# Performance work log

Measured on AMD Instinct MI355X. Metric: run time of the kernel, lower is better.

The kernel has to match this reference:

```python
import jax, jax.numpy as jnp
import numpy as np

N, E, DIN, DH, DOUT = 50000, 800000, 128, 128, 64


def setup_inputs() -> dict:
    key = jax.random.key(0)
    ks = jax.random.split(key, 10)
    s = 0.05  # keep activations numerically sane
    return {
        "x": jax.random.normal(ks[0], (N, DIN), jnp.float32),
        "edge_index": jax.random.randint(ks[1], (2, E), 0, N, jnp.int64),
        "w_in": jax.random.normal(ks[2], (DIN, DH), jnp.float32) * s,
        "b_in": jnp.zeros((DH,), jnp.float32),
        "w_l0": jax.random.normal(ks[3], (DH, DH), jnp.float32) * s,
        "w_r0": jax.random.normal(ks[4], (DH, DH), jnp.float32) * s,
        "b0": jnp.zeros((DH,), jnp.float32),
        "w_l1": jax.random.normal(ks[5], (DH, DH), jnp.float32) * s,
        "w_r1": jax.random.normal(ks[6], (DH, DH), jnp.float32) * s,
        "b1": jnp.zeros((DH,), jnp.float32),
        "w_l2": jax.random.normal(ks[7], (DH, DOUT), jnp.float32) * s,
        "w_r2": jax.random.normal(ks[8], (DH, DOUT), jnp.float32) * s,
        "b2": jnp.zeros((DOUT,), jnp.float32),
    }


def _sage_conv(x, src, dst, w_l, w_r, b, n_nodes):
    # PyG SAGEConv (mean aggr): out = lin_l(mean_{j in N(i)} x_j) + lin_r(x_i)
    msg = x[src]  # [E, d] gather
    agg = jax.ops.segment_sum(msg, dst, num_segments=n_nodes)
    deg = jax.ops.segment_sum(jnp.ones((src.shape[0],), x.dtype), dst, num_segments=n_nodes)
    agg = agg / jnp.maximum(deg, 1.0)[:, None]  # isolated nodes -> 0
    return agg @ w_l + x @ w_r + b


def reference(x, edge_index, w_in, b_in, w_l0, w_r0, b0, w_l1, w_r1, b1, w_l2, w_r2, b2):
    src, dst = edge_index[0], edge_index[1]
    n = x.shape[0]
    h = x @ w_in + b_in
    inp = h
    h = jax.nn.relu(h)
    # conv 0 (hidden->hidden) + relu + (eval dropout = id) + residual
    h = _sage_conv(h, src, dst, w_l0, w_r0, b0, n)
    h = jax.nn.relu(h) + 0.2 * inp
    # conv 1 (hidden->hidden)
    h = _sage_conv(h, src, dst, w_l1, w_r1, b1, n)
    h = jax.nn.relu(h) + 0.2 * inp
    # conv 2 (hidden->out), no activation/residual
    h = _sage_conv(h, src, dst, w_l2, w_r2, b2, n)
    return jax.nn.log_softmax(h, axis=-1)
```

## Files before the change

### kernel.cpp

```cpp
#include <hip/hip_runtime.h>
#include <stdint.h>

#define NN 50000
#define NE 800000
#define NBIN 196
#define ABLK 196
#define EPB 4082
#define BCAP 6144
#define NRT 3125
#define GRID_LIN 1024

typedef __attribute__((ext_vector_type(8))) short short8;
typedef __attribute__((ext_vector_type(4))) float floatx4;

__device__ __forceinline__ uint16_t f2bf(float f){
  union { float f; uint32_t u; } c; c.f = f;
  uint32_t u = c.u + 0x7FFFu + ((c.u >> 16) & 1u);
  return (uint16_t)(u >> 16);
}
__device__ __forceinline__ float bflo(uint32_t v){
  union { uint32_t u; float f; } c; c.u = v << 16; return c.f;
}
__device__ __forceinline__ float bfhi(uint32_t v){
  union { uint32_t u; float f; } c; c.u = v & 0xFFFF0000u; return c.f;
}

#define B_HIST ABLK
#define B_PIN 64
#define B_P0  128
#define B_P1  128
#define B_P2  64

__device__ __forceinline__ void pack_one(int idx, const float* __restrict__ wl,
                                         const float* __restrict__ wr,
                                         uint16_t* __restrict__ bp,
                                         int ncolL, int ncolR, int NT){
  int j = idx & 7, lane = (idx >> 3) & 63, rest = idx >> 9;
  int nt = rest % NT, kt = rest / NT;
  int k = kt * 32 + ((lane >> 4) << 3) + j;
  int n = nt * 16 + (lane & 15);
  float v = (n < ncolL) ? wl[k * ncolL + n] : wr[k * ncolR + (n - ncolL)];
  bp[idx] = f2bf(v);
}

__global__ __launch_bounds__(256) void k_prep(const int* __restrict__ ei, int* __restrict__ histC,
                                              const float* __restrict__ w_in,
                                              const float* __restrict__ w_l0, const float* __restrict__ w_r0,
                                              const float* __restrict__ w_l1, const float* __restrict__ w_r1,
                                              const float* __restrict__ w_l2, const float* __restrict__ w_r2,
                                              uint16_t* __restrict__ bpIn, uint16_t* __restrict__ bp0,
                                              uint16_t* __restrict__ bp1, uint16_t* __restrict__ bp2){
  __shared__ int hsh[NBIN];
  int b = blockIdx.x;
  if (b < B_HIST){
    for (int i = threadIdx.x; i < NBIN; i += 256) hsh[i] = 0;
    __syncthreads();
    int base = b * EPB;
    for (int k = threadIdx.x; k < EPB; k += 256){
      int e = base + k;
      if (e < NE) atomicAdd(&hsh[ei[NE + e] >> 8], 1);
    }
    __syncthreads();
    for (int i = threadIdx.x; i < NBIN; i += 256) histC[b * NBIN + i] = hsh[i];
    return;
  }
  b -= B_HIST;
  if (b < B_PIN){ pack_one(b * 256 + threadIdx.x, w_in, w_in, bpIn, 128, 0, 8); return; }
  b -= B_PIN;
  if (b < B_P0){ pack_one(b * 256 + threadIdx.x, w_l0, w_r0, bp0, 128, 128, 16); return; }
  b -= B_P0;
  if (b < B_P1){ pack_one(b * 256 + threadIdx.x, w_l1, w_r1, bp1, 128, 128, 16); return; }
  b -= B_P1;
  pack_one(b * 256 + threadIdx.x, w_l2, w_r2, bp2, 64, 64, 8);
}

__global__ __launch_bounds__(256) void k_scanS1(const int* __restrict__ histC, int* __restrict__ histE,
                                                int* __restrict__ colTot){
  __shared__ int s[256];
  int t = blockIdx.x;
  int b = threadIdx.x;
  int v = (b < ABLK) ? histC[b * NBIN + t] : 0;
  s[b] = v;
  __syncthreads();
  #pragma unroll
  for (int off = 1; off < 256; off <<= 1){
    int u = (b >= off) ? s[b - off] : 0;
    __syncthreads();
    s[b] += u;
    __syncthreads();
  }
  if (b < ABLK) histE[b * NBIN + t] = s[b] - v;
  if (b == ABLK - 1) colTot[t] = s[b];
}

__global__ __launch_bounds__(256) void k_scanS2(const int* __restrict__ colTot, int* __restrict__ binStart){
  __shared__ int s[256];
  int t = threadIdx.x;
  int tot = (t < NBIN) ? colTot[t] : 0;
  s[t] = tot;
  __syncthreads();
  #pragma unroll
  for (int off = 1; off < 256; off <<= 1){
    int u = (t >= off) ? s[t - off] : 0;
    __syncthreads();
    s[t] += u;
    __syncthreads();
  }
  if (t < NBIN) binStart[t] = s[t] - tot;
  if (t == 0) binStart[NBIN] = NE;
}

#define B_BIN 196
#define SMSZ 20488

__global__ __launch_bounds__(256) void k_mid(const int* __restrict__ ei,
                                             const int* __restrict__ histC, const int* __restrict__ histE,
                                             const int* __restrict__ binStart,
                                             uint32_t* __restrict__ pairs,
                                             const float* __restrict__ x,
                                             const uint16_t* __restrict__ BpIn, const float* __restrict__ b_in,
                                             const uint16_t* __restrict__ Bp0, const float* __restrict__ b0,
                                             uint16_t* __restrict__ resb, uint16_t* __restrict__ y0,
                                             uint16_t* __restrict__ z0){
  __shared__ __align__(16) char smraw[SMSZ];
  int t = threadIdx.x;
  if (blockIdx.x < B_BIN){
    int* loc = (int*)smraw;
    int* cur = loc + NBIN;
    int* gof = cur + NBIN;
    int* sc  = gof + NBIN + NBIN;
    uint32_t* st = (uint32_t*)(sc + 256);
    int b = blockIdx.x;
    int cv = (t < NBIN) ? histC[b * NBIN + t] : 0;
    sc[t] = cv;
    __syncthreads();
    #pragma unroll
    for (int off = 1; off < 256; off <<= 1){
      int u = (t >= off) ? sc[t - off] : 0;
      __syncthreads();
      sc[t] += u;
      __syncthreads();
    }
    if (t < NBIN){
      int excl = sc[t] - cv;
      loc[t] = excl;
      cur[t] = excl;
      gof[t] = binStart[t] + histE[b * NBIN + t];
    }
    __syncthreads();
    int base = b * EPB;
    for (int k = t; k < EPB; k += 256){
      int e = base + k;
      if (e < NE){
        int d = ei[NE + e];
        int s0 = ei[e];
        int pos = atomicAdd(&cur[d >> 8], 1);
        st[pos] = (uint32_t)s0 | ((uint32_t)d << 16);
      }
    }
    __syncthreads();
    int cnt = min(EPB, NE - base);
    for (int k = t; k < cnt; k += 256){
      uint32_t v = st[k];
      int bin = (int)(v >> 24);
      pairs[gof[bin] + (k - loc[bin])] = v;
    }
    return;
  }
  uint16_t* ash = (uint16_t*)smraw;
  int lane = t & 63, wave = t >> 6;
  short8 bIn[4][2], bC0[4][4];
  #pragma unroll
  for (int kt = 0; kt < 4; ++kt){
    #pragma unroll
    for (int n = 0; n < 2; ++n)
      bIn[kt][n] = *(const short8*)(BpIn + (size_t)((kt * 8 + wave * 2 + n) * 64 + lane) * 8);
    #pragma unroll
    for (int n = 0; n < 4; ++n)
      bC0[kt][n] = *(const short8*)(Bp0 + (size_t)((kt * 16 + wave * 4 + n) * 64 + lane) * 8);
  }
  int m = lane & 15, quad = lane >> 4;
  for (int rt = blockIdx.x - B_BIN; rt < NRT; rt += GRID_LIN){
    int r0 = rt * 16;
    const float* xrow = x + (size_t)(r0 + m) * 128 + quad * 8;
    short8 af[4];
    #pragma unroll
    for (int kt = 0; kt < 4; ++kt){
      float4 p = *(const float4*)(xrow + kt * 32);
      float4 q2 = *(const float4*)(xrow + kt * 32 + 4);
      short8 a;
      a[0] = (short)f2bf(p.x);  a[1] = (short)f2bf(p.y);
      a[2] = (short)f2bf(p.z);  a[3] = (short)f2bf(p.w);
      a[4] = (short)f2bf(q2.x); a[5] = (short)f2bf(q2.y);
      a[6] = (short)f2bf(q2.z); a[7] = (short)f2bf(q2.w);
      af[kt] = a;
    }
    floatx4 accH[2];
    #pragma unroll
    for (int n = 0; n < 2; ++n) accH[n] = (floatx4){0.f, 0.f, 0.f, 0.f};
    #pragma unroll
    for (int kt = 0; kt < 4; ++kt)
      #pragma unroll
      for (int n = 0; n < 2; ++n)
        accH[n] = __builtin_amdgcn_mfma_f32_16x16x32_bf16(af[kt], bIn[kt][n], accH[n], 0, 0, 0);
    int rbase = r0 + quad * 4;
    __syncthreads();
    #pragma unroll
    for (int n = 0; n < 2; ++n){
      int c = (wave * 2 + n) * 16 + m;
      float bi = b_in[c];
      #pragma unroll
      for (int i = 0; i < 4; ++i){
        float hh = accH[n][i] + bi;
        int row = rbase + i;
        resb[(size_t)row * 128 + c] = f2bf(0.2f * hh);
        ash[(quad * 4 + i) * 136 + c] = f2bf(fmaxf(hh, 0.f));
      }
    }
    __syncthreads();
    short8 af2[4];
    #pragma unroll
    for (int kt = 0; kt < 4; ++kt)
      af2[kt] = *(const short8*)&ash[m * 136 + quad * 8 + kt * 32];
    floatx4 acc[4];
    #pragma unroll
    for (int n = 0; n < 4; ++n) acc[n] = (floatx4){0.f, 0.f, 0.f, 0.f};
    #pragma unroll
    for (int kt = 0; kt < 4; ++kt)
      #pragma unroll
      for (int n = 0; n < 4; ++n)
        acc[n] = __builtin_amdgcn_mfma_f32_16x16x32_bf16(af2[kt], bC0[kt][n], acc[n], 0, 0, 0);
    #pragma unroll
    for (int n = 0; n < 4; ++n){
      int c = (wave * 4 + n) * 16 + m;
      #pragma unroll
      for (int i = 0; i < 4; ++i){
        float v = acc[n][i];
        int row = rbase + i;
        if (c < 128) y0[(size_t)row * 128 + c] = f2bf(v);
        else         z0[(size_t)row * 128 + (c - 128)] = f2bf(v + b0[c - 128]);
      }
    }
  }
}

__global__ __launch_bounds__(256) void k_csr(const uint32_t* __restrict__ pairs, const int* __restrict__ binStart,
                                             int* __restrict__ rowp, uint16_t* __restrict__ colx){
  __shared__ uint32_t pl[BCAP];
  __shared__ uint16_t stg[BCAP];
  __shared__ int h[256], sc[256];
  int i = blockIdx.x, t = threadIdx.x;
  int p0 = binStart[i], p1 = binStart[i + 1];
  int cnt = min(p1 - p0, BCAP);
  for (int k = t; k < cnt; k += 256) pl[k] = pairs[p0 + k];
  h[t] = 0;
  __syncthreads();
  for (int k = t; k < cnt; k += 256) atomicAdd(&h[(pl[k] >> 16) & 255], 1);
  __syncthreads();
  int cv = h[t];
  sc[t] = cv;
  __syncthreads();
  #pragma unroll
  for (int off = 1; off < 256; off <<= 1){
    int u = (t >= off) ? sc[t - off] : 0;
    __syncthreads();
    sc[t] += u;
    __syncthreads();
  }
  int excl = sc[t] - cv;
  int n0 = i << 8;
  int nc = min(256, NN - n0);
  if (t < nc) rowp[n0 + t] = p0 + excl;
  if (i == NBIN - 1 && t == 0) rowp[NN] = NE;
  h[t] = excl;
  __syncthreads();
  for (int k = t; k < cnt; k += 256){
    uint32_t v = pl[k];
    int pos = atomicAdd(&h[(v >> 16) & 255], 1);
    stg[pos] = (uint16_t)(v & 0xFFFFu);
  }
  __syncthreads();
  for (int k = t; k < cnt; k += 256) colx[p0 + k] = stg[k];
}

template<int NTW, int MODE>
__global__ __launch_bounds__(256) void k_gemm(const uint16_t* __restrict__ A, const uint16_t* __restrict__ Bp,
                                              const float* __restrict__ bias,
                                              uint16_t* __restrict__ o0, uint16_t* __restrict__ o1,
                                              float* __restrict__ o2){
  const int NTT = 4 * NTW;
  int lane = threadIdx.x & 63;
  int wave = threadIdx.x >> 6;
  short8 bfrag[4][NTW];
  #pragma unroll
  for (int kt = 0; kt < 4; ++kt)
    #pragma unroll
    for (int n = 0; n < NTW; ++n)
      bfrag[kt][n] = *(const short8*)(Bp + (size_t)((kt * NTT + wave * NTW + n) * 64 + lane) * 8);

  int m = lane & 15, quad = lane >> 4;
  const int nrt = NN / 16;
  for (int rt = blockIdx.x; rt < nrt; rt += gridDim.x){
    int r0 = rt * 16;
    const uint16_t* arow = A + (size_t)(r0 + m) * 128 + quad * 8;
    short8 af[4];
    #pragma unroll
    for (int kt = 0; kt < 4; ++kt) af[kt] = *(const short8*)(arow + kt * 32);
    floatx4 acc[NTW];
    #pragma unroll
    for (int n = 0; n < NTW; ++n) acc[n] = (floatx4){0.f, 0.f, 0.f, 0.f};
    #pragma unroll
    for (int kt = 0; kt < 4; ++kt)
      #pragma unroll
      for (int n = 0; n < NTW; ++n)
        acc[n] = __builtin_amdgcn_mfma_f32_16x16x32_bf16(af[kt], bfrag[kt][n], acc[n], 0, 0, 0);

    int rbase = r0 + quad * 4;
    #pragma unroll
    for (int n = 0; n < NTW; ++n){
      int c = (wave * NTW + n) * 16 + m;
      #pragma unroll
      for (int i = 0; i < 4; ++i){
        float v = acc[n][i];
        int row = rbase + i;
        if (MODE == 1){
          if (c < 128) o0[(size_t)row * 128 + c] = f2bf(v);
          else         o1[(size_t)row * 128 + (c - 128)] = f2bf(v + bias[c - 128]);
        } else {
          if (c < 64) o0[(size_t)row * 64 + c] = f2bf(v);
          else        o2[(size_t)row * 64 + (c - 64)] = v + bias[c - 64];
        }
      }
    }
  }
}

__global__ __launch_bounds__(256) void agg_mid(const uint4* __restrict__ yb, const uint4* __restrict__ zb,
                                               const uint4* __restrict__ resb,
                                               const uint16_t* __restrict__ colx, const int* __restrict__ rowp,
                                               uint4* __restrict__ hb_out){
  int wid = blockIdx.x * 4 + (threadIdx.x >> 6);
  if (wid >= NN) return;
  int lane = threadIdx.x & 63;
  int q = lane >> 4, sub = lane & 15;
  int e0 = rowp[wid], e1 = rowp[wid + 1];
  float a0 = 0.f, a1 = 0.f, a2 = 0.f, a3 = 0.f, a4 = 0.f, a5 = 0.f, a6 = 0.f, a7 = 0.f;
  int e = e0 + q;
  for (; e + 12 < e1; e += 16){
    uint4 v0 = yb[(size_t)colx[e]      * 16 + sub];
    uint4 v1 = yb[(size_t)colx[e + 4]  * 16 + sub];
    uint4 v2 = yb[(size_t)colx[e + 8]  * 16 + sub];
    uint4 v3 = yb[(size_t)colx[e + 12] * 16 + sub];
    a0 += bflo(v0.x) + bflo(v1.x) + bflo(v2.x) + bflo(v3.x);
    a1 += bfhi(v0.x) + bfhi(v1.x) + bfhi(v2.x) + bfhi(v3.x);
    a2 += bflo(v0.y) + bflo(v1.y) + bflo(v2.y) + bflo(v3.y);
    a3 += bfhi(v0.y) + bfhi(v1.y) + bfhi(v2.y) + bfhi(v3.y);
    a4 += bflo(v0.z) + bflo(v1.z) + bflo(v2.z) + bflo(v3.z);
    a5 += bfhi(v0.z) + bfhi(v1.z) + bfhi(v2.z) + bfhi(v3.z);
    a6 += bflo(v0.w) + bflo(v1.w) + bflo(v2.w) + bflo(v3.w);
    a7 += bfhi(v0.w) + bfhi(v1.w) + bfhi(v2.w) + bfhi(v3.w);
  }
  for (; e < e1; e += 4){
    uint4 v = yb[(size_t)colx[e] * 16 + sub];
    a0 += bflo(v.x); a1 += bfhi(v.x); a2 += bflo(v.y); a3 += bfhi(v.y);
    a4 += bflo(v.z); a5 += bfhi(v.z); a6 += bflo(v.w); a7 += bfhi(v.w);
  }
  #pragma unroll
  for (int off = 16; off < 64; off <<= 1){
    a0 += __shfl_xor(a0, off, 64);
    a1 += __shfl_xor(a1, off, 64);
    a2 += __shfl_xor(a2, off, 64);
    a3 += __shfl_xor(a3, off, 64);
    a4 += __shfl_xor(a4, off, 64);
    a5 += __shfl_xor(a5, off, 64);
    a6 += __shfl_xor(a6, off, 64);
    a7 += __shfl_xor(a7, off, 64);
  }
  int deg = e1 - e0;
  float inv = deg > 0 ? 1.f / (float)deg : 0.f;
  if (q == 0){
    uint4 zv = zb[(size_t)wid * 16 + sub];
    uint4 rv = resb[(size_t)wid * 16 + sub];
    float w0 = fmaxf(a0 * inv + bflo(zv.x), 0.f) + bflo(rv.x);
    float w1 = fmaxf(a1 * inv + bfhi(zv.x), 0.f) + bfhi(rv.x);
    float w2 = fmaxf(a2 * inv + bflo(zv.y), 0.f) + bflo(rv.y);
    float w3 = fmaxf(a3 * inv + bfhi(zv.y), 0.f) + bfhi(rv.y);
    float w4 = fmaxf(a4 * inv + bflo(zv.z), 0.f) + bflo(rv.z);
    float w5 = fmaxf(a5 * inv + bfhi(zv.z), 0.f) + bfhi(rv.z);
    float w6 = fmaxf(a6 * inv + bflo(zv.w), 0.f) + bflo(rv.w);
    float w7 = fmaxf(a7 * inv + bfhi(zv.w), 0.f) + bfhi(rv.w);
    uint4 o;
    o.x = (uint32_t)f2bf(w0) | ((uint32_t)f2bf(w1) << 16);
    o.y = (uint32_t)f2bf(w2) | ((uint32_t)f2bf(w3) << 16);
    o.z = (uint32_t)f2bf(w4) | ((uint32_t)f2bf(w5) << 16);
    o.w = (uint32_t)f2bf(w6) | ((uint32_t)f2bf(w7) << 16);
    hb_out[(size_t)wid * 16 + sub] = o;
  }
}

__global__ __launch_bounds__(256) void agg_out(const uint2* __restrict__ yb2, const float* __restrict__ z2,
                                               const uint16_t* __restrict__ colx, const int* __restrict__ rowp,
                                               float* __restrict__ out){
  int wid = blockIdx.x * 4 + (threadIdx.x >> 6);
  if (wid >= NN) return;
  int lane = threadIdx.x & 63;
  int q = lane >> 4, sub = lane & 15;
  int e0 = rowp[wid], e1 = rowp[wid + 1];
  float a0 = 0.f, a1 = 0.f, a2 = 0.f, a3 = 0.f;
  int e = e0 + q;
  for (; e + 12 < e1; e += 16){
    uint2 v0 = yb2[(size_t)colx[e]      * 16 + sub];
    uint2 v1 = yb2[(size_t)colx[e + 4]  * 16 + sub];
    uint2 v2 = yb2[(size_t)colx[e + 8]  * 16 + sub];
    uint2 v3 = yb2[(size_t)colx[e + 12] * 16 + sub];
    a0 += bflo(v0.x) + bflo(v1.x) + bflo(v2.x) + bflo(v3.x);
    a1 += bfhi(v0.x) + bfhi(v1.x) + bfhi(v2.x) + bfhi(v3.x);
    a2 += bflo(v0.y) + bflo(v1.y) + bflo(v2.y) + bflo(v3.y);
    a3 += bfhi(v0.y) + bfhi(v1.y) + bfhi(v2.y) + bfhi(v3.y);
  }
  for (; e < e1; e += 4){
    uint2 v = yb2[(size_t)colx[e] * 16 + sub];
    a0 += bflo(v.x); a1 += bfhi(v.x); a2 += bflo(v.y); a3 += bfhi(v.y);
  }
  #pragma unroll
  for (int off = 16; off < 64; off <<= 1){
    a0 += __shfl_xor(a0, off, 64);
    a1 += __shfl_xor(a1, off, 64);
    a2 += __shfl_xor(a2, off, 64);
    a3 += __shfl_xor(a3, off, 64);
  }
  int deg = e1 - e0;
  float inv = deg > 0 ? 1.f / (float)deg : 0.f;
  float4 zv = ((const float4*)z2)[(size_t)wid * 16 + sub];
  float v0 = a0 * inv + zv.x;
  float v1 = a1 * inv + zv.y;
  float v2 = a2 * inv + zv.z;
  float v3 = a3 * inv + zv.w;
  float mx = fmaxf(fmaxf(v0, v1), fmaxf(v2, v3));
  #pragma unroll
  for (int off = 1; off < 16; off <<= 1) mx = fmaxf(mx, __shfl_xor(mx, off, 64));
  float sm = __expf(v0 - mx) + __expf(v1 - mx) + __expf(v2 - mx) + __expf(v3 - mx);
  #pragma unroll
  for (int off = 1; off < 16; off <<= 1) sm += __shfl_xor(sm, off, 64);
  if (q == 0){
    float ls = __logf(sm);
    float4 o = make_float4((v0 - mx) - ls, (v1 - mx) - ls, (v2 - mx) - ls, (v3 - mx) - ls);
    ((float4*)out)[(size_t)wid * 16 + sub] = o;
  }
}

extern "C" void kernel_launch(void* const* d_in, const int* in_sizes, int n_in,
                              void* d_out, int out_size, void* d_ws, size_t ws_size,
                              hipStream_t stream){
  const float* x    = (const float*)d_in[0];
  const int*   ei   = (const int*)d_in[1];
  const float* w_in = (const float*)d_in[2];
  const float* b_in = (const float*)d_in[3];
  const float* w_l0 = (const float*)d_in[4];
  const float* w_r0 = (const float*)d_in[5];
  const float* b0   = (const float*)d_in[6];
  const float* w_l1 = (const float*)d_in[7];
  const float* w_r1 = (const float*)d_in[8];
  const float* b1   = (const float*)d_in[9];
  const float* w_l2 = (const float*)d_in[10];
  const float* w_r2 = (const float*)d_in[11];
  const float* b2   = (const float*)d_in[12];
  float* out = (float*)d_out;

  char* ws = (char*)d_ws;
  size_t off = 0;
  auto take = [&](size_t bytes) -> char* {
    char* p = ws + off;
    off = (off + bytes + 1023) & ~(size_t)1023;
    return p;
  };
  uint16_t* hb   = (uint16_t*)take((size_t)NN * 128 * 2);
  uint16_t* resb = (uint16_t*)take((size_t)NN * 128 * 2);
  uint16_t* y0   = (uint16_t*)take((size_t)NN * 128 * 2);
  uint16_t* z0   = (uint16_t*)take((size_t)NN * 128 * 2);
  uint32_t* pairs = (uint32_t*)take((size_t)NE * 4);
  uint16_t* colx  = (uint16_t*)take((size_t)NE * 2);
  int* histC    = (int*)take((size_t)NBIN * ABLK * 4);
  int* histE    = (int*)take((size_t)NBIN * ABLK * 4);
  int* colTot   = (int*)take((size_t)NBIN * 4);
  int* binStart = (int*)take((size_t)(NBIN + 1) * 4);
  int* rowp     = (int*)take((size_t)(NN + 1) * 4);
  uint16_t* BpIn = (uint16_t*)take(128 * 128 * 2);
  uint16_t* Bp0  = (uint16_t*)take(128 * 256 * 2);
  uint16_t* Bp1  = (uint16_t*)take(128 * 256 * 2);
  uint16_t* Bp2  = (uint16_t*)take(128 * 128 * 2);
  uint16_t* y2 = y0;
  float*    z2 = (float*)z0;
  (void)ws_size; (void)in_sizes; (void)n_in; (void)out_size;

  k_prep<<<B_HIST + B_PIN + B_P0 + B_P1 + B_P2, 256, 0, stream>>>(
      ei, histC, w_in, w_l0, w_r0, w_l1, w_r1, w_l2, w_r2, BpIn, Bp0, Bp1, Bp2);

  k_scanS1<<<NBIN, 256, 0, stream>>>(histC, histE, colTot);
  k_scanS2<<<1, 256, 0, stream>>>(colTot, binStart);

  k_mid<<<B_BIN + GRID_LIN, 256, 0, stream>>>(ei, histC, histE, binStart, pairs, x,
                                              BpIn, b_in, Bp0, b0, resb, y0, z0);

  k_csr<<<NBIN, 256, 0, stream>>>(pairs, binStart, rowp, colx);

  agg_mid<<<NN / 4, 256, 0, stream>>>((const uint4*)y0, (const uint4*)z0, (const uint4*)resb,
                                      colx, rowp, (uint4*)hb);
  k_gemm<4, 1><<<1024, 256, 0, stream>>>(hb, Bp1, b1, y0, z0, nullptr);

  agg_mid<<<NN / 4, 256, 0, stream>>>((const uint4*)y0, (const uint4*)z0, (const uint4*)resb,
                                      colx, rowp, (uint4*)hb);
  k_gemm<2, 2><<<1024, 256, 0, stream>>>(hb, Bp2, b2, y2, nullptr, z2);

  agg_out<<<NN / 4, 256, 0, stream>>>((const uint2*)y2, z2, colx, rowp, out);
}
```

Baseline: 277.0 us.

## Split fused bin/linear kernel and stage GEMM outputs through LDS for coalesced stores

The fused k_mid kernel, which mixed edge binning and the input/conv0 linear layers in one launch, is split into separate k_bin and k_lin0 kernels. All the dense GEMM kernels (lin0, gemm1, gemm2) now write MFMA results into padded shared-memory tiles and then emit full-row 16-byte vector stores, replacing scattered 2-byte per-element global writes. This aims to cut uncoalesced write traffic. It costs an extra kernel launch, the loss of overlap between binning and the GEMM, and extra barriers per tile.

```diff
diff --git a/kernel.cpp b/kernel.cpp
--- a/kernel.cpp
+++ b/kernel.cpp
@@ -8,7 +8,7 @@
 #define EPB 4082
 #define BCAP 6144
 #define NRT 3125
-#define GRID_LIN 1024
+#define GRID_G 1024
 
 typedef __attribute__((ext_vector_type(8))) short short8;
 typedef __attribute__((ext_vector_type(4))) float floatx4;
@@ -110,64 +110,59 @@
   if (t == 0) binStart[NBIN] = NE;
 }
 
-#define B_BIN 196
-#define SMSZ 20488
-
-__global__ __launch_bounds__(256) void k_mid(const int* __restrict__ ei,
+__global__ __launch_bounds__(256) void k_bin(const int* __restrict__ ei,
                                              const int* __restrict__ histC, const int* __restrict__ histE,
                                              const int* __restrict__ binStart,
-                                             uint32_t* __restrict__ pairs,
-                                             const float* __restrict__ x,
-                                             const uint16_t* __restrict__ BpIn, const float* __restrict__ b_in,
-                                             const uint16_t* __restrict__ Bp0, const float* __restrict__ b0,
-                                             uint16_t* __restrict__ resb, uint16_t* __restrict__ y0,
-                                             uint16_t* __restrict__ z0){
-  __shared__ __align__(16) char smraw[SMSZ];
+                                             uint32_t* __restrict__ pairs){
+  __shared__ int loc[NBIN], cur[NBIN], gof[NBIN];
+  __shared__ int sc[256];
+  __shared__ uint32_t st[EPB];
   int t = threadIdx.x;
-  if (blockIdx.x < B_BIN){
-    int* loc = (int*)smraw;
-    int* cur = loc + NBIN;
-    int* gof = cur + NBIN;
-    int* sc  = gof + NBIN + NBIN;
-    uint32_t* st = (uint32_t*)(sc + 256);
-    int b = blockIdx.x;
-    int cv = (t < NBIN) ? histC[b * NBIN + t] : 0;
-    sc[t] = cv;
-    __syncthreads();
-    #pragma unroll
-    for (int off = 1; off < 256; off <<= 1){
-      int u = (t >= off) ? sc[t - off] : 0;
-      __syncthreads();
-      sc[t] += u;
-      __syncthreads();
-    }
-    if (t < NBIN){
-      int excl = sc[t] - cv;
-      loc[t] = excl;
-      cur[t] = excl;
-      gof[t] = binStart[t] + histE[b * NBIN + t];
-    }
-    __syncthreads();
-    int base = b * EPB;
-    for (int k = t; k < EPB; k += 256){
-      int e = base + k;
-      if (e < NE){
-        int d = ei[NE + e];
-        int s0 = ei[e];
-        int pos = atomicAdd(&cur[d >> 8], 1);
-        st[pos] = (uint32_t)s0 | ((uint32_t)d << 16);
-      }
-    }
-    __syncthreads();
-    int cnt = min(EPB, NE - base);
-    for (int k = t; k < cnt; k += 256){
-      uint32_t v = st[k];
-      int bin = (int)(v >> 24);
-      pairs[gof[bin] + (k - loc[bin])] = v;
-    }
-    return;
-  }
-  uint16_t* ash = (uint16_t*)smraw;
+  int b = blockIdx.x;
+  int cv = (t < NBIN) ? histC[b * NBIN + t] : 0;
+  sc[t] = cv;
+  __syncthreads();
+  #pragma unroll
+  for (int off = 1; off < 256; off <<= 1){
+    int u = (t >= off) ? sc[t - off] : 0;
+    __syncthreads();
+    sc[t] += u;
+    __syncthreads();
+  }
+  if (t < NBIN){
+    int excl = sc[t] - cv;
+    loc[t] = excl;
+    cur[t] = excl;
+    gof[t] = binStart[t] + histE[b * NBIN + t];
+  }
+  __syncthreads();
+  int base = b * EPB;
+  for (int k = t; k < EPB; k += 256){
+    int e = base + k;
+    if (e < NE){
+      int d = ei[NE + e];
+      int s0 = ei[e];
+      int pos = atomicAdd(&cur[d >> 8], 1);
+      st[pos] = (uint32_t)s0 | ((uint32_t)d << 16);
+    }
+  }
+  __syncthreads();
+  int cnt = min(EPB, NE - base);
+  for (int k = t; k < cnt; k += 256){
+    uint32_t v = st[k];
+    int bin = (int)(v >> 24);
+    pairs[gof[bin] + (k - loc[bin])] = v;
+  }
+}
+
+__global__ __launch_bounds__(256) void k_lin0(const float* __restrict__ x,
+                                              const uint16_t* __restrict__ BpIn, const float* __restrict__ b_in,
+                                              const uint16_t* __restrict__ Bp0, const float* __restrict__ b0,
+                                              uint16_t* __restrict__ resb, uint16_t* __restrict__ y0,
+                                              uint16_t* __restrict__ z0){
+  __shared__ uint16_t smA[16 * 136];
+  __shared__ uint16_t smB[16 * 136];
+  int t = threadIdx.x;
   int lane = t & 63, wave = t >> 6;
   short8 bIn[4][2], bC0[4][4];
   #pragma unroll
@@ -180,7 +175,8 @@
       bC0[kt][n] = *(const short8*)(Bp0 + (size_t)((kt * 16 + wave * 4 + n) * 64 + lane) * 8);
   }
   int m = lane & 15, quad = lane >> 4;
-  for (int rt = blockIdx.x - B_BIN; rt < NRT; rt += GRID_LIN){
+  int orow = t >> 4, ochunk = t & 15;
+  for (int rt = blockIdx.x; rt < NRT; rt += GRID_G){
     int r0 = rt * 16;
     const float* xrow = x + (size_t)(r0 + m) * 128 + quad * 8;
     short8 af[4];
@@ -203,7 +199,6 @@
       #pragma unroll
       for (int n = 0; n < 2; ++n)
         accH[n] = __builtin_amdgcn_mfma_f32_16x16x32_bf16(af[kt], bIn[kt][n], accH[n], 0, 0, 0);
-    int rbase = r0 + quad * 4;
     __syncthreads();
     #pragma unroll
     for (int n = 0; n < 2; ++n){
@@ -212,16 +207,17 @@
       #pragma unroll
       for (int i = 0; i < 4; ++i){
         float hh = accH[n][i] + bi;
-        int row = rbase + i;
-        resb[(size_t)row * 128 + c] = f2bf(0.2f * hh);
-        ash[(quad * 4 + i) * 136 + c] = f2bf(fmaxf(hh, 0.f));
+        int row = quad * 4 + i;
+        smA[row * 136 + c] = f2bf(fmaxf(hh, 0.f));
+        smB[row * 136 + c] = f2bf(0.2f * hh);
       }
     }
     __syncthreads();
+    *((uint4*)(resb + (size_t)(r0 + orow) * 128) + ochunk) = *(const uint4*)&smB[orow * 136 + ochunk * 8];
     short8 af2[4];
     #pragma unroll
     for (int kt = 0; kt < 4; ++kt)
-      af2[kt] = *(const short8*)&ash[m * 136 + quad * 8 + kt * 32];
+      af2[kt] = *(const short8*)&smA[m * 136 + quad * 8 + kt * 32];
     floatx4 acc[4];
     #pragma unroll
     for (int n = 0; n < 4; ++n) acc[n] = (floatx4){0.f, 0.f, 0.f, 0.f};
@@ -230,17 +226,21 @@
       #pragma unroll
       for (int n = 0; n < 4; ++n)
         acc[n] = __builtin_amdgcn_mfma_f32_16x16x32_bf16(af2[kt], bC0[kt][n], acc[n], 0, 0, 0);
+    __syncthreads();
     #pragma unroll
     for (int n = 0; n < 4; ++n){
       int c = (wave * 4 + n) * 16 + m;
       #pragma unroll
       for (int i = 0; i < 4; ++i){
         float v = acc[n][i];
-        int row = rbase + i;
-        if (c < 128) y0[(size_t)row * 128 + c] = f2bf(v);
-        else         z0[(size_t)row * 128 + (c - 128)] = f2bf(v + b0[c - 128]);
+        int row = quad * 4 + i;
+        if (c < 128) smA[row * 136 + c] = f2bf(v);
+        else         smB[row * 136 + (c - 128)] = f2bf(v + b0[c - 128]);
       }
     }
+    __syncthreads();
+    *((uint4*)(y0 + (size_t)(r0 + orow) * 128) + ochunk) = *(const uint4*)&smA[orow * 136 + ochunk * 8];
+    *((uint4*)(z0 + (size_t)(r0 + orow) * 128) + ochunk) = *(const uint4*)&smB[orow * 136 + ochunk * 8];
   }
 }
 
@@ -283,54 +283,101 @@
   for (int k = t; k < cnt; k += 256) colx[p0 + k] = stg[k];
 }
 
-template<int NTW, int MODE>
-__global__ __launch_bounds__(256) void k_gemm(const uint16_t* __restrict__ A, const uint16_t* __restrict__ Bp,
-                                              const float* __restrict__ bias,
-                                              uint16_t* __restrict__ o0, uint16_t* __restrict__ o1,
-                                              float* __restrict__ o2){
-  const int NTT = 4 * NTW;
-  int lane = threadIdx.x & 63;
-  int wave = threadIdx.x >> 6;
-  short8 bfrag[4][NTW];
+__global__ __launch_bounds__(256) void k_gemm1(const uint16_t* __restrict__ A, const uint16_t* __restrict__ Bp,
+                                               const float* __restrict__ bias,
+                                               uint16_t* __restrict__ o0, uint16_t* __restrict__ o1){
+  __shared__ uint16_t smY[16 * 136];
+  __shared__ uint16_t smZ[16 * 136];
+  int t = threadIdx.x;
+  int lane = t & 63, wave = t >> 6;
+  short8 bfrag[4][4];
   #pragma unroll
   for (int kt = 0; kt < 4; ++kt)
     #pragma unroll
-    for (int n = 0; n < NTW; ++n)
-      bfrag[kt][n] = *(const short8*)(Bp + (size_t)((kt * NTT + wave * NTW + n) * 64 + lane) * 8);
-
+    for (int n = 0; n < 4; ++n)
+      bfrag[kt][n] = *(const short8*)(Bp + (size_t)((kt * 16 + wave * 4 + n) * 64 + lane) * 8);
   int m = lane & 15, quad = lane >> 4;
-  const int nrt = NN / 16;
-  for (int rt = blockIdx.x; rt < nrt; rt += gridDim.x){
+  int orow = t >> 4, ochunk = t & 15;
+  for (int rt = blockIdx.x; rt < NRT; rt += GRID_G){
     int r0 = rt * 16;
     const uint16_t* arow = A + (size_t)(r0 + m) * 128 + quad * 8;
     short8 af[4];
     #pragma unroll
     for (int kt = 0; kt < 4; ++kt) af[kt] = *(const short8*)(arow + kt * 32);
-    floatx4 acc[NTW];
-    #pragma unroll
-    for (int n = 0; n < NTW; ++n) acc[n] = (floatx4){0.f, 0.f, 0.f, 0.f};
+    floatx4 acc[4];
+    #pragma unroll
+    for (int n = 0; n < 4; ++n) acc[n] = (floatx4){0.f, 0.f, 0.f, 0.f};
     #pragma unroll
     for (int kt = 0; kt < 4; ++kt)
       #pragma unroll
-      for (int n = 0; n < NTW; ++n)
+      for (int n = 0; n < 4; ++n)
         acc[n] = __builtin_amdgcn_mfma_f32_16x16x32_bf16(af[kt], bfrag[kt][n], acc[n], 0, 0, 0);
-
-    int rbase = r0 + quad * 4;
-    #pragma unroll
-    for (int n = 0; n < NTW; ++n){
-      int c = (wave * NTW + n) * 16 + m;
+    __syncthreads();
+    #pragma unroll
+    for (int n = 0; n < 4; ++n){
+      int c = (wave * 4 + n) * 16 + m;
       #pragma unroll
       for (int i = 0; i < 4; ++i){
         float v = acc[n][i];
-        int row = rbase + i;
-        if (MODE == 1){
-          if (c < 128) o0[(size_t)row * 128 + c] = f2bf(v);
-          else         o1[(size_t)row * 128 + (c - 128)] = f2bf(v + bias[c - 128]);
-        } else {
-          if (c < 64) o0[(size_t)row * 64 + c] = f2bf(v);
-          else        o2[(size_t)row * 64 + (c - 64)] = v + bias[c - 64];
-        }
+        int row = quad * 4 + i;
+        if (c < 128) smY[row * 136 + c] = f2bf(v);
+        else         smZ[row * 136 + (c - 128)] = f2bf(v + bias[c - 128]);
       }
+    }
+    __syncthreads();
+    *((uint4*)(o0 + (size_t)(r0 + orow) * 128) + ochunk) = *(const uint4*)&smY[orow * 136 + ochunk * 8];
+    *((uint4*)(o1 + (size_t)(r0 + orow) * 128) + ochunk) = *(const uint4*)&smZ[orow * 136 + ochunk * 8];
+  }
+}
+
+__global__ __launch_bounds__(256) void k_gemm2(const uint16_t* __restrict__ A, const uint16_t* __restrict__ Bp,
+                                               const float* __restrict__ bias,
+                                               uint16_t* __restrict__ o0, float* __restrict__ o2){
+  __shared__ uint16_t smY[16 * 72];
+  __shared__ float smZ[16 * 68];
+  int t = threadIdx.x;
+  int lane = t & 63, wave = t >> 6;
+  short8 bfrag[4][2];
+  #pragma unroll
+  for (int kt = 0; kt < 4; ++kt)
+    #pragma unroll
+    for (int n = 0; n < 2; ++n)
+      bfrag[kt][n] = *(const short8*)(Bp + (size_t)((kt * 8 + wave * 2 + n) * 64 + lane) * 8);
+  int m = lane & 15, quad = lane >> 4;
+  for (int rt = blockIdx.x; rt < NRT; rt += GRID_G){
+    int r0 = rt * 16;
+    const uint16_t* arow = A + (size_t)(r0 + m) * 128 + quad * 8;
+    short8 af[4];
+    #pragma unroll
+    for (int kt = 0; kt < 4; ++kt) af[kt] = *(const short8*)(arow + kt * 32);
+    floatx4 acc[2];
+    #pragma unroll
+    for (int n = 0; n < 2; ++n) acc[n] = (floatx4){0.f, 0.f, 0.f, 0.f};
+    #pragma unroll
+    for (int kt = 0; kt < 4; ++kt)
+      #pragma unroll
+      for (int n = 0; n < 2; ++n)
+        acc[n] = __builtin_amdgcn_mfma_f32_16x16x32_bf16(af[kt], bfrag[kt][n], acc[n], 0, 0, 0);
+    __syncthreads();
+    #pragma unroll
+    for (int n = 0; n < 2; ++n){
+      int c = (wave * 2 + n) * 16 + m;
+      #pragma unroll
+      for (int i = 0; i < 4; ++i){
+        float v = acc[n][i];
+        int row = quad * 4 + i;
+        if (c < 64) smY[row * 72 + c] = f2bf(v);
+        else        smZ[row * 68 + (c - 64)] = v + bias[c - 64];
+      }
+    }
+    __syncthreads();
+    if (t < 128){
+      int row = t >> 3, chunk = t & 7;
+      *((uint4*)(o0 + (size_t)(r0 + row) * 64) + chunk) = *(const uint4*)&smY[row * 72 + chunk * 8];
+    }
+    {
+      int row = t >> 4, chunk = t & 15;
+      *((uint4*)(o2 + (size_t)(r0 + row) * 64) + chunk) = *(const uint4*)&smZ[row * 68 + chunk * 4];
     }
   }
 }
@@ -499,18 +546,18 @@
   k_scanS1<<<NBIN, 256, 0, stream>>>(histC, histE, colTot);
   k_scanS2<<<1, 256, 0, stream>>>(colTot, binStart);
 
-  k_mid<<<B_BIN + GRID_LIN, 256, 0, stream>>>(ei, histC, histE, binStart, pairs, x,
-                                              BpIn, b_in, Bp0, b0, resb, y0, z0);
-
+  k_lin0<<<GRID_G, 256, 0, stream>>>(x, BpIn, b_in, Bp0, b0, resb, y0, z0);
+
+  k_bin<<<ABLK, 256, 0, stream>>>(ei, histC, histE, binStart, pairs);
   k_csr<<<NBIN, 256, 0, stream>>>(pairs, binStart, rowp, colx);
 
   agg_mid<<<NN / 4, 256, 0, stream>>>((const uint4*)y0, (const uint4*)z0, (const uint4*)resb,
                                       colx, rowp, (uint4*)hb);
-  k_gemm<4, 1><<<1024, 256, 0, stream>>>(hb, Bp1, b1, y0, z0, nullptr);
+  k_gemm1<<<GRID_G, 256, 0, stream>>>(hb, Bp1, b1, y0, z0);
 
   agg_mid<<<NN / 4, 256, 0, stream>>>((const uint4*)y0, (const uint4*)z0, (const uint4*)resb,
                                       colx, rowp, (uint4*)hb);
-  k_gemm<2, 2><<<1024, 256, 0, stream>>>(hb, Bp2, b2, y2, nullptr, z2);
+  k_gemm2<<<GRID_G, 256, 0, stream>>>(hb, Bp2, b2, y2, z2);
 
   agg_out<<<NN / 4, 256, 0, stream>>>((const uint2*)y2, z2, colx, rowp, out);
 }
```

New measurement: 289.1 us. 4.4% more time.
